# Kernel optimization log

Hardware: AMD Instinct MI355X
Metric: run time of the kernel (lower is better)

## Reference

```python
import jax, jax.numpy as jnp
import numpy as np

P = 14  # chain length, hard-coded by edge_index construction (range(14))
B = 4096
BN_EPS = 1e-5
ALPHA = 1.0
DIMS = [(3, 64), (64, 64), (64, 64), (64, 128), (128, 1024)]


def setup_inputs() -> dict:
    key = jax.random.key(0)
    ks = jax.random.split(key, 40)
    inp = {}
    inp["x1"] = jax.random.normal(ks[0], (B, 3, P), jnp.float32)
    inp["x2"] = jax.random.normal(ks[1], (B, 3, P), jnp.float32)
    for li, (din, dout) in enumerate(DIMS, 1):
        inp[f"W{li}"] = jax.random.normal(ks[1 + li], (din, dout), jnp.float32) / np.float32(np.sqrt(din))
        inp[f"b{li}"] = jnp.zeros((dout,), jnp.float32)
        inp[f"gamma{li}"] = jnp.ones((dout,), jnp.float32)
        inp[f"beta{li}"] = jnp.zeros((dout,), jnp.float32)
    inp["emb_W"] = jax.random.normal(ks[10], (1024, 10), jnp.float32) / np.float32(32.0)
    inp["emb_b"] = jnp.zeros((10,), jnp.float32)
    inp["clu_W"] = jax.random.normal(ks[11], (800, 10), jnp.float32) * np.float32(0.1)  # xavier-ish
    return inp


def _chain_agg(h):
    # h: [B*P, d]; equivalent to A @ h where A is the block-diagonal chain
    # adjacency (i<->i+1, no self-loops) built by the original Python loop.
    h3 = h.reshape(B, P, -1)
    agg = (jnp.pad(h3[:, 1:], ((0, 0), (0, 1), (0, 0)))
           + jnp.pad(h3[:, :-1], ((0, 0), (1, 0), (0, 0))))
    return agg.reshape(B * P, -1)


def _gcn_block(h, W, b, gamma, beta):
    # GCNConv: A @ (X W) + b ; then BatchNorm1d (training stats) ; ReLU
    h = _chain_agg(h @ W) + b
    mu = h.mean(axis=0)
    var = ((h - mu) ** 2).mean(axis=0)  # biased var, as torch BN uses for normalization
    h = gamma * (h - mu) * jax.lax.rsqrt(var + BN_EPS) + beta
    return jax.nn.relu(h)


def _forward_single(x, params):
    # x: [B, 3, P] -> [B, P, 3] -> [B*P, 3]
    h = jnp.transpose(x, (0, 2, 1)).reshape(B * P, 3)
    for li in range(1, 6):
        h = _gcn_block(h, params[f"W{li}"], params[f"b{li}"], params[f"gamma{li}"], params[f"beta{li}"])
    h = h.reshape(B, P, -1).max(axis=1)            # [B, 1024]
    extra = h @ params["emb_W"] + params["emb_b"]  # [B, 10]
    # ClusterlingLayer (Student-t assignment)
    d = jnp.sum((extra[:, None, :] - params["clu_W"]) ** 2, axis=2)  # [B, 800]
    q = (1.0 + d / ALPHA) ** (-(ALPHA + 1.0) / 2.0)
    q = q / q.sum(axis=1, keepdims=True)
    return q, extra, d


def reference(x1, x2, W1, b1, gamma1, beta1, W2, b2, gamma2, beta2,
              W3, b3, gamma3, beta3, W4, b4, gamma4, beta4,
              W5, b5, gamma5, beta5, emb_W, emb_b, clu_W):
    params = dict(W1=W1, b1=b1, gamma1=gamma1, beta1=beta1,
                  W2=W2, b2=b2, gamma2=gamma2, beta2=beta2,
                  W3=W3, b3=b3, gamma3=gamma3, beta3=beta3,
                  W4=W4, b4=b4, gamma4=gamma4, beta4=beta4,
                  W5=W5, b5=b5, gamma5=gamma5, beta5=beta5,
                  emb_W=emb_W, emb_b=emb_b, clu_W=clu_W)
    c1, e1, d1 = _forward_single(x1, params)
    c2, e2, d2 = _forward_single(x2, params)
    sim = jnp.linalg.norm(e1 - e2 + 1e-6, axis=1)  # torch pairwise_distance eps
    return sim, c1, c2, e1, e2, d1
```

## Files before the change

### kernel.cpp

```cpp
#include <hip/hip_runtime.h>
#include <hip/hip_bf16.h>

#define NB 4096
#define PLEN 14
#define NROWS (NB*PLEN)
#define BN_EPS 1e-5f

#define SLOT_STRIDE 32768
#define INP_STRIDE  133120
#define SLOT5_OFF   131072
#define NBANK 16

typedef __bf16 bf16x8 __attribute__((ext_vector_type(8)));
typedef float  f32x4  __attribute__((ext_vector_type(4)));

__global__ __launch_bounds__(256) void wprep_kernel(
    const float* __restrict__ W2, const float* __restrict__ W3,
    const float* __restrict__ W4, const float* __restrict__ W5,
    __bf16* __restrict__ wt2, __bf16* __restrict__ wt3,
    __bf16* __restrict__ wt4, __bf16* __restrict__ wt5b,
    float* __restrict__ stats)
{
    int idx = blockIdx.x*256 + threadIdx.x;
    if (idx < 2*INP_STRIDE) { stats[idx] = 0.f; return; }
    idx -= 2*INP_STRIDE;
    if (idx < 4096) { int n = idx>>6, k = idx&63; wt2[idx] = (__bf16)W2[k*64+n]; return; }
    idx -= 4096;
    if (idx < 4096) { int n = idx>>6, k = idx&63; wt3[idx] = (__bf16)W3[k*64+n]; return; }
    idx -= 4096;
    if (idx < 8192) { int n = idx>>6, k = idx&63; wt4[idx] = (__bf16)W4[k*128+n]; return; }
    idx -= 8192;
    int kk = idx & 7, n = (idx >> 3) & 63, kg = (idx >> 9) & 15, c = idx >> 13;
    wt5b[idx] = (__bf16)W5[(kg*8 + kk)*1024 + c*64 + n];
}

__global__ __launch_bounds__(256) void l1_kernel(
    const float* __restrict__ x1,
    const float* __restrict__ x2,
    const float* __restrict__ W,
    const float* __restrict__ bias,
    __bf16* __restrict__ pre,
    float* __restrict__ stats)
{
    const int col  = threadIdx.x & 63;
    const int sub  = threadIdx.x >> 6;
    const int chain = blockIdx.x * 4 + sub;
    const int inp  = chain >> 12;
    const int bank = blockIdx.x & (NBANK-1);
    const float w0 = W[0*64+col], w1 = W[1*64+col], w2 = W[2*64+col];
    const float bb = bias[col];
    const float* xb = (inp ? x2 : x1) + (chain & 4095)*3*PLEN;
    float s = 0.f, s2 = 0.f;
    for (int p = 0; p < PLEN; p++) {
        float u0 = 0.f, u1 = 0.f, u2 = 0.f;
        if (p > 0)      { u0 += xb[p-1]; u1 += xb[PLEN+p-1]; u2 += xb[2*PLEN+p-1]; }
        if (p < PLEN-1) { u0 += xb[p+1]; u1 += xb[PLEN+p+1]; u2 += xb[2*PLEN+p+1]; }
        float v = u0*w0 + u1*w1 + u2*w2 + bb;
        pre[(size_t)(chain*PLEN + p)*64 + col] = (__bf16)v;
        s += v; s2 += v*v;
    }
    __shared__ float ss[4][64], ssq[4][64];
    ss[sub][col] = s; ssq[sub][col] = s2;
    __syncthreads();
    if (sub == 0) {
        float ts  = ss[0][col]+ss[1][col]+ss[2][col]+ss[3][col];
        float ts2 = ssq[0][col]+ssq[1][col]+ssq[2][col]+ssq[3][col];
        float* st = stats + inp*INP_STRIDE + bank*2048;
        atomicAdd(&st[col], ts);
        atomicAdd(&st[1024 + col], ts2);
    }
}

template<int NOUT>
__global__ __launch_bounds__(256) void layer_kernel(
    const __bf16* __restrict__ prev,
    const float* __restrict__ stats_in,
    const float* __restrict__ gamma, const float* __restrict__ beta,
    const __bf16* __restrict__ wt,
    const float* __restrict__ bias,
    __bf16* __restrict__ outp,
    float* __restrict__ stats_out)
{
    constexpr int KP = 72;
    constexpr int NCH = NOUT/64;
    __shared__ __align__(16) short sA[112*KP];
    const int tid = threadIdx.x, wave = tid >> 6, lane = tid & 63;
    const int m = lane & 15, q = lane >> 4;
    const int rowbase = blockIdx.x * 112;
    const int soff = (blockIdx.x >> 9) * INP_STRIDE;
    const int bank = blockIdx.x & (NBANK-1);
    const float* sin_ = stats_in + soff;

    bf16x8 breg[NCH][2];
    #pragma unroll
    for (int cc = 0; cc < NCH; ++cc)
        #pragma unroll
        for (int ksi = 0; ksi < 2; ++ksi)
            breg[cc][ksi] = *reinterpret_cast<const bf16x8*>(
                wt + (cc*64 + wave*16 + m)*64 + ksi*32 + q*8);

    {
        const int ch = tid >> 5, c2 = (tid & 31)*2;
        float s0 = 0.f, q0 = 0.f, s1 = 0.f, q1 = 0.f;
        #pragma unroll
        for (int bk = 0; bk < NBANK; ++bk) {
            s0 += sin_[bk*2048 + c2];
            q0 += sin_[bk*2048 + 1024 + c2];
            s1 += sin_[bk*2048 + c2 + 1];
            q1 += sin_[bk*2048 + 1024 + c2 + 1];
        }
        float mu0 = s0*(1.f/NROWS);
        float v0  = q0*(1.f/NROWS) - mu0*mu0;
        float a0  = gamma[c2]*rsqrtf(v0+BN_EPS), c0 = beta[c2]-mu0*a0;
        float mu1 = s1*(1.f/NROWS);
        float v1  = q1*(1.f/NROWS) - mu1*mu1;
        float a1  = gamma[c2+1]*rsqrtf(v1+BN_EPS), c1 = beta[c2+1]-mu1*a1;
        float h0[14], h1[14];
        const __bf16* src = prev + (size_t)(rowbase + ch*14)*64 + c2;
        #pragma unroll
        for (int r = 0; r < 14; ++r) {
            union { unsigned u; __bf16 b[2]; } ld;
            ld.u = *reinterpret_cast<const unsigned*>(src + r*64);
            h0[r] = fmaxf(a0*(float)ld.b[0] + c0, 0.f);
            h1[r] = fmaxf(a1*(float)ld.b[1] + c1, 0.f);
        }
        #pragma unroll
        for (int r = 0; r < 14; ++r) {
            float g0 = (r>0 ? h0[r-1] : 0.f) + (r<13 ? h0[r+1] : 0.f);
            float g1 = (r>0 ? h1[r-1] : 0.f) + (r<13 ? h1[r+1] : 0.f);
            union { __bf16 b[2]; unsigned u; } pk;
            pk.b[0] = (__bf16)g0; pk.b[1] = (__bf16)g1;
            *reinterpret_cast<unsigned*>(&sA[(ch*14+r)*KP + c2]) = pk.u;
        }
    }
    __syncthreads();

    f32x4 acc[NCH][7];
    #pragma unroll
    for (int cc = 0; cc < NCH; ++cc)
        #pragma unroll
        for (int t = 0; t < 7; ++t) acc[cc][t] = (f32x4){0.f,0.f,0.f,0.f};

    #pragma unroll
    for (int ksi = 0; ksi < 2; ++ksi) {
        bf16x8 af[7];
        #pragma unroll
        for (int t = 0; t < 7; ++t)
            af[t] = *reinterpret_cast<const bf16x8*>(&sA[(t*16+m)*KP + ksi*32 + q*8]);
        #pragma unroll
        for (int cc = 0; cc < NCH; ++cc)
            #pragma unroll
            for (int t = 0; t < 7; ++t)
                acc[cc][t] = __builtin_amdgcn_mfma_f32_16x16x32_bf16(af[t], breg[cc][ksi], acc[cc][t], 0, 0, 0);
    }

    float* stout = stats_out + soff + bank*2048;
    #pragma unroll
    for (int cc = 0; cc < NCH; ++cc) {
        const int ocol = cc*64 + wave*16 + m;
        const float bb = bias[ocol];
        float s = 0.f, s2 = 0.f;
        #pragma unroll
        for (int t = 0; t < 7; ++t)
            #pragma unroll
            for (int r = 0; r < 4; ++r) {
                float v = acc[cc][t][r] + bb;
                outp[(size_t)(rowbase + t*16 + q*4 + r)*NOUT + ocol] = (__bf16)v;
                s += v; s2 += v*v;
            }
        s  += __shfl_xor(s, 16);  s  += __shfl_xor(s, 32);
        s2 += __shfl_xor(s2, 16); s2 += __shfl_xor(s2, 32);
        if (lane < 16) {
            atomicAdd(&stout[ocol], s);
            atomicAdd(&stout[1024 + ocol], s2);
        }
    }
}

__global__ __launch_bounds__(256, 1) void l5_kernel(
    const __bf16* __restrict__ prev,
    const float* __restrict__ stats_in,
    const float* __restrict__ gamma, const float* __restrict__ beta,
    const __bf16* __restrict__ wtb,
    const float* __restrict__ bias,
    const float* __restrict__ g5,
    __bf16* __restrict__ osel,
    float* __restrict__ part)
{
    __shared__ __align__(16) short sA[112*136];
    const int tid = threadIdx.x, wave = tid >> 6, lane = tid & 63;
    const int m = lane & 15, q = lane >> 4;
    const int rowbase = blockIdx.x * 112;
    const int soff = (blockIdx.x >> 9) * INP_STRIDE;
    const float* sin_ = stats_in + soff;
    float* pb = part + (size_t)blockIdx.x * 2048;

    const char* gw = (const char*)wtb;
    const int boffB = q*1024 + (wave*16 + m)*16;

    bf16x8 bA[4], bB[4];
    #pragma unroll
    for (int k4 = 0; k4 < 4; ++k4)
        bA[k4] = *reinterpret_cast<const bf16x8*>(gw + boffB + k4*4096);

    {
        const int ch = tid >> 5, c4 = (tid & 31)*4;
        float aa[4], cc4[4];
        #pragma unroll
        for (int j = 0; j < 4; ++j) {
            float sb = 0.f, qb = 0.f;
            #pragma unroll
            for (int bk = 0; bk < NBANK; ++bk) {
                sb += sin_[bk*2048 + c4+j];
                qb += sin_[bk*2048 + 1024 + c4+j];
            }
            float mu = sb*(1.f/NROWS);
            float vr = qb*(1.f/NROWS) - mu*mu;
            aa[j] = gamma[c4+j]*rsqrtf(vr+BN_EPS);
            cc4[j] = beta[c4+j] - mu*aa[j];
        }
        float h[14][4];
        const __bf16* src = prev + (size_t)(rowbase + ch*14)*128 + c4;
        #pragma unroll
        for (int r = 0; r < 14; ++r) {
            union { uint2 u; __bf16 b[4]; } ld;
            ld.u = *reinterpret_cast<const uint2*>(src + r*128);
            h[r][0] = fmaxf(aa[0]*(float)ld.b[0] + cc4[0], 0.f);
            h[r][1] = fmaxf(aa[1]*(float)ld.b[1] + cc4[1], 0.f);
            h[r][2] = fmaxf(aa[2]*(float)ld.b[2] + cc4[2], 0.f);
            h[r][3] = fmaxf(aa[3]*(float)ld.b[3] + cc4[3], 0.f);
        }
        const int qq = ch >> 1, jb = (ch & 1) * 14;
        #pragma unroll
        for (int p = 0; p < 14; ++p) {
            int j = jb + p;
            int slot = (j>>2)*16 + qq*4 + (j&3);
            union { __bf16 b[4]; uint2 u; } pk;
            #pragma unroll
            for (int jj = 0; jj < 4; ++jj) {
                float g = (p>0 ? h[p-1][jj] : 0.f) + (p<13 ? h[p+1][jj] : 0.f);
                pk.b[jj] = (__bf16)g;
            }
            *reinterpret_cast<uint2*>(&sA[slot*136 + c4]) = pk.u;
        }
    }
    __syncthreads();

    bf16x8 af[7][4];
    #pragma unroll
    for (int t = 0; t < 7; ++t)
        #pragma unroll
        for (int kk = 0; kk < 4; ++kk)
            af[t][kk] = *reinterpret_cast<const bf16x8*>(&sA[(t*16 + m)*136 + kk*32 + q*8]);

    auto step = [&](int c, bf16x8 (&bR)[4]) {
        f32x4 acc[7];
        #pragma unroll
        for (int t = 0; t < 7; ++t) acc[t] = (f32x4){0.f,0.f,0.f,0.f};
        #pragma unroll
        for (int k4 = 0; k4 < 4; ++k4)
            #pragma unroll
            for (int t = 0; t < 7; ++t)
                acc[t] = __builtin_amdgcn_mfma_f32_16x16x32_bf16(af[t][k4], bR[k4], acc[t], 0, 0, 0);
        const int ocol = c*64 + wave*16 + m;
        const float bb = bias[ocol];
        const float sg = (g5[ocol] >= 0.f) ? 1.f : -1.f;
        float s = 0.f, s2 = 0.f;
        float mx0 = -3.4e38f, mx1 = -3.4e38f;
        #pragma unroll
        for (int t = 0; t < 7; ++t)
            #pragma unroll
            for (int r = 0; r < 4; ++r) {
                float v = acc[t][r] + bb;
                s += v; s2 += v*v;
                float va = sg * v;
                if (t*4 + r < 14) mx0 = fmaxf(mx0, va);
                else              mx1 = fmaxf(mx1, va);
            }
        osel[(size_t)(blockIdx.x*8 + 2*q    )*1024 + ocol] = (__bf16)(sg * mx0);
        osel[(size_t)(blockIdx.x*8 + 2*q + 1)*1024 + ocol] = (__bf16)(sg * mx1);
        s  += __shfl_xor(s, 16);  s  += __shfl_xor(s, 32);
        s2 += __shfl_xor(s2, 16); s2 += __shfl_xor(s2, 32);
        if (lane < 16) {
            pb[ocol]        = s;
            pb[1024 + ocol] = s2;
        }
    };

    #pragma unroll 1
    for (int cc = 0; cc < 16; cc += 2) {
        {
            const char* gb = gw + (size_t)(cc+1)*16384 + boffB;
            #pragma unroll
            for (int k4 = 0; k4 < 4; ++k4)
                bB[k4] = *reinterpret_cast<const bf16x8*>(gb + k4*4096);
        }
        step(cc, bA);
        if (cc + 2 < 16) {
            const char* gb = gw + (size_t)(cc+2)*16384 + boffB;
            #pragma unroll
            for (int k4 = 0; k4 < 4; ++k4)
                bA[k4] = *reinterpret_cast<const bf16x8*>(gb + k4*4096);
        }
        step(cc + 1, bB);
    }
}

__global__ __launch_bounds__(256) void sreduce_kernel(
    const float* __restrict__ part, float* __restrict__ stats)
{
    const int cg  = blockIdx.x*256 + threadIdx.x;
    const int inp = cg >> 11;
    const int col = cg & 2047;
    const float* p = part + (size_t)inp*512*2048 + col;
    float s = 0.f;
    #pragma unroll 4
    for (int b = 0; b < 512; ++b)
        s += p[(size_t)b*2048];
    stats[inp*INP_STRIDE + SLOT5_OFF + col] = s;
}

__global__ __launch_bounds__(256) void headclu_kernel(
    const __bf16* __restrict__ osel,
    const float* __restrict__ stats,
    const float* __restrict__ gamma, const float* __restrict__ beta,
    const float* __restrict__ embW, const float* __restrict__ embB,
    const float* __restrict__ cluW,
    float* __restrict__ e1, float* __restrict__ e2,
    float* __restrict__ c1, float* __restrict__ c2,
    float* __restrict__ d1, float* __restrict__ simOut)
{
    const int b = blockIdx.x, tid = threadIdx.x;
    const int wave = tid >> 6, lane = tid & 63;
    __shared__ float red[4][20];
    __shared__ float se[2][10];
    __shared__ float sred[4][2];

    const float* st0 = stats + SLOT5_OFF;
    const float* st1 = stats + INP_STRIDE + SLOT5_OFF;
    const __bf16* row0 = osel + (size_t)b*1024;
    const __bf16* row1 = osel + (size_t)(NB + b)*1024;

    float acc0[10], acc1[10];
    #pragma unroll
    for (int j = 0; j < 10; ++j) { acc0[j] = 0.f; acc1[j] = 0.f; }
    #pragma unroll
    for (int i = 0; i < 4; ++i) {
        int k = tid + i*256;
        float g = gamma[k], bt = beta[k];
        float mu0 = st0[k]*(1.f/NROWS);
        float va0 = st0[1024+k]*(1.f/NROWS) - mu0*mu0;
        float a0 = g*rsqrtf(va0+BN_EPS);
        float c0 = bt - mu0*a0;
        float mu1 = st1[k]*(1.f/NROWS);
        float va1 = st1[1024+k]*(1.f/NROWS) - mu1*mu1;
        float a1 = g*rsqrtf(va1+BN_EPS);
        float c1_ = bt - mu1*a1;
        float h0 = fmaxf(a0*(float)row0[k] + c0, 0.f);
        float h1 = fmaxf(a1*(float)row1[k] + c1_, 0.f);
        #pragma unroll
        for (int j = 0; j < 10; ++j) {
            float w = embW[k*10 + j];
            acc0[j] += h0 * w;
            acc1[j] += h1 * w;
        }
    }
    #pragma unroll
    for (int j = 0; j < 10; ++j) {
        acc0[j] += __shfl_down(acc0[j], 32);
        acc0[j] += __shfl_down(acc0[j], 16);
        acc0[j] += __shfl_down(acc0[j], 8);
        acc0[j] += __shfl_down(acc0[j], 4);
        acc0[j] += __shfl_down(acc0[j], 2);
        acc0[j] += __shfl_down(acc0[j], 1);
        acc1[j] += __shfl_down(acc1[j], 32);
        acc1[j] += __shfl_down(acc1[j], 16);
        acc1[j] += __shfl_down(acc1[j], 8);
        acc1[j] += __shfl_down(acc1[j], 4);
        acc1[j] += __shfl_down(acc1[j], 2);
        acc1[j] += __shfl_down(acc1[j], 1);
    }
    if (lane == 0)
        #pragma unroll
        for (int j = 0; j < 10; ++j) {
            red[wave][j]      = acc0[j];
            red[wave][10 + j] = acc1[j];
        }
    __syncthreads();
    if (tid < 20) {
        int inp = tid / 10, j = tid % 10;
        float t = red[0][tid]+red[1][tid]+red[2][tid]+red[3][tid] + embB[j];
        se[inp][j] = t;
        (inp ? e2 : e1)[b*10 + j] = t;
    }
    __syncthreads();

    float ev0[10], ev1[10];
    #pragma unroll
    for (int j = 0; j < 10; ++j) { ev0[j] = se[0][j]; ev1[j] = se[1][j]; }
    float d0loc[4], d1loc[4], q0loc[4], q1loc[4], qs0 = 0.f, qs1 = 0.f;
    #pragma unroll
    for (int i = 0; i < 4; ++i) {
        int mm = tid + i*256;
        float dd0 = 0.f, dd1 = 0.f;
        if (mm < 800) {
            #pragma unroll
            for (int j = 0; j < 10; ++j) {
                float cw = cluW[mm*10 + j];
                float t0 = ev0[j] - cw; dd0 += t0*t0;
                float t1 = ev1[j] - cw; dd1 += t1*t1;
            }
        }
        d0loc[i] = dd0; d1loc[i] = dd1;
        float q0v = (mm < 800) ? 1.f/(1.f + dd0) : 0.f;
        float q1v = (mm < 800) ? 1.f/(1.f + dd1) : 0.f;
        q0loc[i] = q0v; q1loc[i] = q1v;
        qs0 += q0v; qs1 += q1v;
    }
    float t0 = qs0, t1 = qs1;
    t0 += __shfl_down(t0,32); t0 += __shfl_down(t0,16); t0 += __shfl_down(t0,8);
    t0 += __shfl_down(t0,4);  t0 += __shfl_down(t0,2);  t0 += __shfl_down(t0,1);
    t1 += __shfl_down(t1,32); t1 += __shfl_down(t1,16); t1 += __shfl_down(t1,8);
    t1 += __shfl_down(t1,4);  t1 += __shfl_down(t1,2);  t1 += __shfl_down(t1,1);
    if (lane == 0) { sred[wave][0] = t0; sred[wave][1] = t1; }
    __syncthreads();
    float inv0 = 1.f / (sred[0][0]+sred[1][0]+sred[2][0]+sred[3][0]);
    float inv1 = 1.f / (sred[0][1]+sred[1][1]+sred[2][1]+sred[3][1]);
    #pragma unroll
    for (int i = 0; i < 4; ++i) {
        int mm = tid + i*256;
        if (mm < 800) {
            c1[(size_t)b*800 + mm] = q0loc[i]*inv0;
            c2[(size_t)b*800 + mm] = q1loc[i]*inv1;
            d1[(size_t)b*800 + mm] = d0loc[i];
        }
    }
    if (tid == 0) {
        float ss = 0.f;
        #pragma unroll
        for (int j = 0; j < 10; ++j) {
            float df = ev0[j] - ev1[j] + 1e-6f;
            ss += df*df;
        }
        simOut[b] = sqrtf(ss);
    }
}

extern "C" void kernel_launch(void* const* d_in, const int* in_sizes, int n_in,
                              void* d_out, int out_size, void* d_ws, size_t ws_size,
                              hipStream_t stream)
{
    const float* x1 = (const float*)d_in[0];
    const float* x2 = (const float*)d_in[1];
    const float *W[5], *bi[5], *ga[5], *be[5];
    for (int l = 0; l < 5; l++) {
        W[l]  = (const float*)d_in[2 + 4*l];
        bi[l] = (const float*)d_in[3 + 4*l];
        ga[l] = (const float*)d_in[4 + 4*l];
        be[l] = (const float*)d_in[5 + 4*l];
    }
    const float* embW = (const float*)d_in[22];
    const float* embB = (const float*)d_in[23];
    const float* cluW = (const float*)d_in[24];
    float* out = (float*)d_out;
    float* ws  = (float*)d_ws;

    float*  stats = ws;
    __bf16* wt2   = (__bf16*)(ws + 2*INP_STRIDE);
    __bf16* wt3   = wt2 + 4096;
    __bf16* wt4   = wt2 + 8192;
    __bf16* wt5b  = wt2 + 16384;
    float*  R1f   = ws + 2*INP_STRIDE + 73728;
    float*  R2f   = R1f + 8388608;
    __bf16* P0    = (__bf16*)R1f;
    __bf16* P1    = (__bf16*)R2f;
    __bf16* Q     = (__bf16*)R2f;
    __bf16* osel  = (__bf16*)R1f;
    float*  part  = R2f + 7340032;

    wprep_kernel<<<1616, 256, 0, stream>>>(W[1], W[2], W[3], W[4],
                                           wt2, wt3, wt4, wt5b, stats);

    float* simO = out;
    float* c1O  = out + 4096;
    float* c2O  = out + 3280896;
    float* e1O  = out + 6557696;
    float* e2O  = out + 6598656;
    float* d1O  = out + 6639616;

    l1_kernel<<<2048, 256, 0, stream>>>(x1, x2, W[0], bi[0], P0, stats);
    layer_kernel<64><<<1024, 256, 0, stream>>>(
        P0, stats + 0*SLOT_STRIDE, ga[0], be[0], wt2, bi[1], P1, stats + 1*SLOT_STRIDE);
    layer_kernel<64><<<1024, 256, 0, stream>>>(
        P1, stats + 1*SLOT_STRIDE, ga[1], be[1], wt3, bi[2], P0, stats + 2*SLOT_STRIDE);
    layer_kernel<128><<<1024, 256, 0, stream>>>(
        P0, stats + 2*SLOT_STRIDE, ga[2], be[2], wt4, bi[3], Q, stats + 3*SLOT_STRIDE);
    l5_kernel<<<1024, 256, 0, stream>>>(
        Q, stats + 3*SLOT_STRIDE, ga[3], be[3], wt5b, bi[4], ga[4], osel, part);
    sreduce_kernel<<<16, 256, 0, stream>>>(part, stats);
    headclu_kernel<<<4096, 256, 0, stream>>>(
        osel, stats, ga[4], be[4], embW, embB, cluW,
        e1O, e2O, c1O, c2O, d1O, simO);
}
```

Before: 288.0 us.

## Halve rows per block in GCN layers and split stats reduction across more blocks

Layers 2-4 now process 56 rows (4 sequences) per block instead of 112, doubling the grid to 2048 blocks and shrinking shared memory and accumulator registers. The MFMA tile is padded to 64 rows with zeroed LDS rows, and the output writes skip the padding. The layer-5 stats reduction is split into 16 slices per column and combined with atomics, running on 256 blocks instead of 16. Padding wastes about an eighth of the MFMA work, and the extra blocks add more stat atomics. This relies on the stats buffer having been zeroed beforehand.

Measured after the change: 249.9 us. 13.2% less time.

```diff
diff --git a/kernel.cpp b/kernel.cpp
--- a/kernel.cpp
+++ b/kernel.cpp
@@ -83,11 +83,11 @@
 {
     constexpr int KP = 72;
     constexpr int NCH = NOUT/64;
-    __shared__ __align__(16) short sA[112*KP];
+    __shared__ __align__(16) short sA[64*KP];
     const int tid = threadIdx.x, wave = tid >> 6, lane = tid & 63;
     const int m = lane & 15, q = lane >> 4;
-    const int rowbase = blockIdx.x * 112;
-    const int soff = (blockIdx.x >> 9) * INP_STRIDE;
+    const int rowbase = blockIdx.x * 56;
+    const int soff = (blockIdx.x >> 10) * INP_STRIDE;
     const int bank = blockIdx.x & (NBANK-1);
     const float* sin_ = stats_in + soff;
 
@@ -99,58 +99,53 @@
             breg[cc][ksi] = *reinterpret_cast<const bf16x8*>(
                 wt + (cc*64 + wave*16 + m)*64 + ksi*32 + q*8);
 
+    #pragma unroll
+    for (int i = tid; i < 512; i += 256) {
+        int rr = 56 + (i >> 6), cc = i & 63;
+        sA[rr*KP + cc] = 0;
+    }
     {
-        const int ch = tid >> 5, c2 = (tid & 31)*2;
-        float s0 = 0.f, q0 = 0.f, s1 = 0.f, q1 = 0.f;
+        const int ch = tid >> 6, c = tid & 63;
+        float sb = 0.f, qb = 0.f;
         #pragma unroll
         for (int bk = 0; bk < NBANK; ++bk) {
-            s0 += sin_[bk*2048 + c2];
-            q0 += sin_[bk*2048 + 1024 + c2];
-            s1 += sin_[bk*2048 + c2 + 1];
-            q1 += sin_[bk*2048 + 1024 + c2 + 1];
-        }
-        float mu0 = s0*(1.f/NROWS);
-        float v0  = q0*(1.f/NROWS) - mu0*mu0;
-        float a0  = gamma[c2]*rsqrtf(v0+BN_EPS), c0 = beta[c2]-mu0*a0;
-        float mu1 = s1*(1.f/NROWS);
-        float v1  = q1*(1.f/NROWS) - mu1*mu1;
-        float a1  = gamma[c2+1]*rsqrtf(v1+BN_EPS), c1 = beta[c2+1]-mu1*a1;
-        float h0[14], h1[14];
-        const __bf16* src = prev + (size_t)(rowbase + ch*14)*64 + c2;
+            sb += sin_[bk*2048 + c];
+            qb += sin_[bk*2048 + 1024 + c];
+        }
+        float mu = sb*(1.f/NROWS);
+        float vr = qb*(1.f/NROWS) - mu*mu;
+        float a = gamma[c]*rsqrtf(vr+BN_EPS), c0 = beta[c]-mu*a;
+        float h[14];
+        const __bf16* src = prev + (size_t)(rowbase + ch*14)*64 + c;
+        #pragma unroll
+        for (int r = 0; r < 14; ++r)
+            h[r] = fmaxf(a*(float)src[r*64] + c0, 0.f);
         #pragma unroll
         for (int r = 0; r < 14; ++r) {
-            union { unsigned u; __bf16 b[2]; } ld;
-            ld.u = *reinterpret_cast<const unsigned*>(src + r*64);
-            h0[r] = fmaxf(a0*(float)ld.b[0] + c0, 0.f);
-            h1[r] = fmaxf(a1*(float)ld.b[1] + c1, 0.f);
-        }
-        #pragma unroll
-        for (int r = 0; r < 14; ++r) {
-            float g0 = (r>0 ? h0[r-1] : 0.f) + (r<13 ? h0[r+1] : 0.f);
-            float g1 = (r>0 ? h1[r-1] : 0.f) + (r<13 ? h1[r+1] : 0.f);
-            union { __bf16 b[2]; unsigned u; } pk;
-            pk.b[0] = (__bf16)g0; pk.b[1] = (__bf16)g1;
-            *reinterpret_cast<unsigned*>(&sA[(ch*14+r)*KP + c2]) = pk.u;
+            float g = (r>0 ? h[r-1] : 0.f) + (r<13 ? h[r+1] : 0.f);
+            union { __bf16 b; short s; } pk;
+            pk.b = (__bf16)g;
+            sA[(ch*14+r)*KP + c] = pk.s;
         }
     }
     __syncthreads();
 
-    f32x4 acc[NCH][7];
+    f32x4 acc[NCH][4];
     #pragma unroll
     for (int cc = 0; cc < NCH; ++cc)
         #pragma unroll
-        for (int t = 0; t < 7; ++t) acc[cc][t] = (f32x4){0.f,0.f,0.f,0.f};
+        for (int t = 0; t < 4; ++t) acc[cc][t] = (f32x4){0.f,0.f,0.f,0.f};
 
     #pragma unroll
     for (int ksi = 0; ksi < 2; ++ksi) {
-        bf16x8 af[7];
-        #pragma unroll
-        for (int t = 0; t < 7; ++t)
+        bf16x8 af[4];
+        #pragma unroll
+        for (int t = 0; t < 4; ++t)
             af[t] = *reinterpret_cast<const bf16x8*>(&sA[(t*16+m)*KP + ksi*32 + q*8]);
         #pragma unroll
         for (int cc = 0; cc < NCH; ++cc)
             #pragma unroll
-            for (int t = 0; t < 7; ++t)
+            for (int t = 0; t < 4; ++t)
                 acc[cc][t] = __builtin_amdgcn_mfma_f32_16x16x32_bf16(af[t], breg[cc][ksi], acc[cc][t], 0, 0, 0);
     }
 
@@ -161,13 +156,15 @@
         const float bb = bias[ocol];
         float s = 0.f, s2 = 0.f;
         #pragma unroll
-        for (int t = 0; t < 7; ++t)
+        for (int t = 0; t < 4; ++t) {
+            if (t == 3 && q >= 2) continue;
             #pragma unroll
             for (int r = 0; r < 4; ++r) {
                 float v = acc[cc][t][r] + bb;
                 outp[(size_t)(rowbase + t*16 + q*4 + r)*NOUT + ocol] = (__bf16)v;
                 s += v; s2 += v*v;
             }
+        }
         s  += __shfl_xor(s, 16);  s  += __shfl_xor(s, 32);
         s2 += __shfl_xor(s2, 16); s2 += __shfl_xor(s2, 32);
         if (lane < 16) {
@@ -309,15 +306,17 @@
 __global__ __launch_bounds__(256) void sreduce_kernel(
     const float* __restrict__ part, float* __restrict__ stats)
 {
-    const int cg  = blockIdx.x*256 + threadIdx.x;
-    const int inp = cg >> 11;
-    const int col = cg & 2047;
-    const float* p = part + (size_t)inp*512*2048 + col;
+    const int g = blockIdx.x*256 + threadIdx.x;
+    const int slice = g >> 12;
+    const int pair  = g & 4095;
+    const int inp = pair >> 11;
+    const int col = pair & 2047;
+    const float* p = part + (size_t)inp*512*2048 + (size_t)slice*32*2048 + col;
     float s = 0.f;
     #pragma unroll 4
-    for (int b = 0; b < 512; ++b)
+    for (int b = 0; b < 32; ++b)
         s += p[(size_t)b*2048];
-    stats[inp*INP_STRIDE + SLOT5_OFF + col] = s;
+    atomicAdd(&stats[inp*INP_STRIDE + SLOT5_OFF + col], s);
 }
 
 __global__ __launch_bounds__(256) void headclu_kernel(
@@ -489,15 +488,15 @@
     float* d1O  = out + 6639616;
 
     l1_kernel<<<2048, 256, 0, stream>>>(x1, x2, W[0], bi[0], P0, stats);
-    layer_kernel<64><<<1024, 256, 0, stream>>>(
+    layer_kernel<64><<<2048, 256, 0, stream>>>(
         P0, stats + 0*SLOT_STRIDE, ga[0], be[0], wt2, bi[1], P1, stats + 1*SLOT_STRIDE);
-    layer_kernel<64><<<1024, 256, 0, stream>>>(
+    layer_kernel<64><<<2048, 256, 0, stream>>>(
         P1, stats + 1*SLOT_STRIDE, ga[1], be[1], wt3, bi[2], P0, stats + 2*SLOT_STRIDE);
-    layer_kernel<128><<<1024, 256, 0, stream>>>(
+    layer_kernel<128><<<2048, 256, 0, stream>>>(
         P0, stats + 2*SLOT_STRIDE, ga[2], be[2], wt4, bi[3], Q, stats + 3*SLOT_STRIDE);
     l5_kernel<<<1024, 256, 0, stream>>>(
         Q, stats + 3*SLOT_STRIDE, ga[3], be[3], wt5b, bi[4], ga[4], osel, part);
-    sreduce_kernel<<<16, 256, 0, stream>>>(part, stats);
+    sreduce_kernel<<<256, 256, 0, stream>>>(part, stats);
     headclu_kernel<<<4096, 256, 0, stream>>>(
         osel, stats, ga[4], be[4], embW, embB, cluW,
         e1O, e2O, c1O, c2O, d1O, simO);
```
